# Optimization experiments

Measured on AMD Instinct MI355X. Metric: run time of the kernel, lower is better.

The kernel has to match this reference:

```python
import jax, jax.numpy as jnp
import numpy as np

N_NODES = 100000
N_EDGES = 1600000
NFEAT, NHID, NCLASS = 128, 64, 40
NLAYERS = 4
P = 2.0


def setup_inputs() -> dict:
    key = jax.random.key(0)
    ks = jax.random.split(key, 10)
    x = jax.random.normal(ks[0], (N_NODES, NFEAT), dtype=jnp.float32)
    edge_index = jax.random.randint(ks[1], (2, N_EDGES), 0, N_NODES, dtype=jnp.int32)
    s_in = 1.0 / np.sqrt(NFEAT)
    s_h = 1.0 / np.sqrt(NHID)
    return {
        "x": x,
        "edge_index": edge_index,
        "enc_W": jax.random.normal(ks[2], (NHID, NFEAT), dtype=jnp.float32) * s_in,
        "enc_b": jnp.zeros((NHID,), dtype=jnp.float32),
        "conv_W": jax.random.normal(ks[3], (NHID, NHID), dtype=jnp.float32) * s_h,
        "conv_b": jnp.zeros((NHID,), dtype=jnp.float32),
        "W_skip": jax.random.normal(ks[4], (NHID, NHID), dtype=jnp.float32) * s_h,
        "dec_W": jax.random.normal(ks[5], (NCLASS, NHID), dtype=jnp.float32) * s_h,
        "dec_b": jnp.zeros((NCLASS,), dtype=jnp.float32),
    }


def _gcn_conv(X, W, b, src, dst, n):
    # PyG GCNConv: add self-loops, symmetric normalization, then X @ W^T + b
    H = X @ W.T  # [n, nhid]
    ones = jnp.ones_like(dst, dtype=X.dtype)
    deg = jax.ops.segment_sum(ones, dst, num_segments=n)  # in-degree incl. self loops
    dinv = jnp.where(deg > 0, jax.lax.rsqrt(deg), 0.0)
    norm = dinv[src] * dinv[dst]  # [E+n]
    out = jax.ops.segment_sum(norm[:, None] * H[src], dst, num_segments=n)
    return out + b


def _gamma(X, row, col, n, p):
    # G2 gating: scatter-mean over edges of sum |X[row]-X[col]|^p, then tanh.
    # (conv_gg output in the original G2 is dead code and omitted.)
    diff = jnp.sum(jnp.abs(X[row] - X[col]) ** p, axis=-1)  # [E]
    s = jax.ops.segment_sum(diff, row, num_segments=n)
    cnt = jax.ops.segment_sum(jnp.ones_like(diff), row, num_segments=n)
    return jnp.tanh(s / jnp.maximum(cnt, 1.0))  # [n]


def reference(x, edge_index, enc_W, enc_b, conv_W, conv_b, W_skip, dec_W, dec_b):
    n = x.shape[0]
    row, col = edge_index[0], edge_index[1]
    # self-loop augmented edges for GCNConv
    loop = jnp.arange(n, dtype=edge_index.dtype)
    src_sl = jnp.concatenate([row, loop])
    dst_sl = jnp.concatenate([col, loop])

    X = jax.nn.relu(x @ enc_W.T + enc_b)  # [n, nhid]
    X_init = X
    skip_val = X_init @ W_skip.T  # constant across layers

    for _ in range(NLAYERS):
        X_agg = jax.nn.relu(_gcn_conv(X, conv_W, conv_b, src_sl, dst_sl, n))
        g = _gamma(X, row, col, n, P)[:, None]  # gamma_smooth == gamma_squash (dead convs)
        denom = 1.0 + g + g
        A = 1.0 / denom
        B = g / denom
        C = g / denom
        X = A * X + B * X_agg + C * skip_val

    return X @ dec_W.T + dec_b  # [n, nclass]
```

## Files before the change

### kernel.cpp

```cpp
#include <hip/hip_runtime.h>
#include <hip/hip_bf16.h>

#define NFEAT 128
#define NHID  64
#define NCLASS 40
#define NLAYERS 4


__global__ void count_rank_k(const int* __restrict__ ei, int E,
                             int* __restrict__ cnt_col, int* __restrict__ cnt_row,
                             int* __restrict__ rank) {
    int t = blockIdx.x * blockDim.x + threadIdx.x;
    int base = t * 4;
    if (base >= E) return;
    if (base + 4 <= E) {
        int4 c4 = *reinterpret_cast<const int4*>(ei + E + base);
        int4 r4 = *reinterpret_cast<const int4*>(ei + base);
        int4 k4;
        k4.x = atomicAdd(&cnt_col[c4.x], 1);
        k4.y = atomicAdd(&cnt_col[c4.y], 1);
        k4.z = atomicAdd(&cnt_col[c4.z], 1);
        k4.w = atomicAdd(&cnt_col[c4.w], 1);
        atomicAdd(&cnt_row[r4.x], 1);
        atomicAdd(&cnt_row[r4.y], 1);
        atomicAdd(&cnt_row[r4.z], 1);
        atomicAdd(&cnt_row[r4.w], 1);
        *reinterpret_cast<int4*>(rank + base) = k4;
    } else {
        for (int e = base; e < E; ++e) {
            rank[e] = atomicAdd(&cnt_col[ei[E + e]], 1);
            atomicAdd(&cnt_row[ei[e]], 1);
        }
    }
}

__global__ void scanA_k(const int* __restrict__ cnt, int* __restrict__ off,
                        int* __restrict__ bsum, float* __restrict__ dinv, int n) {
    __shared__ int t[1024];
    int i = blockIdx.x * 1024 + threadIdx.x;
    int x = (i < n) ? cnt[i] : 0;
    if (i < n) dinv[i] = 1.0f / sqrtf((float)(x + 1));
    t[threadIdx.x] = x;
    __syncthreads();
    for (int d = 1; d < 1024; d <<= 1) {
        int y = (threadIdx.x >= (unsigned)d) ? t[threadIdx.x - d] : 0;
        __syncthreads();
        t[threadIdx.x] += y;
        __syncthreads();
    }
    if (i < n) off[i] = t[threadIdx.x] - x;
    if (threadIdx.x == 1023) bsum[blockIdx.x] = t[1023];
}

__global__ void scanB_k(int* __restrict__ bsum, int nb) {
    __shared__ int t[1024];
    int x = (threadIdx.x < (unsigned)nb) ? bsum[threadIdx.x] : 0;
    t[threadIdx.x] = x;
    __syncthreads();
    for (int d = 1; d < 1024; d <<= 1) {
        int y = (threadIdx.x >= (unsigned)d) ? t[threadIdx.x - d] : 0;
        __syncthreads();
        t[threadIdx.x] += y;
        __syncthreads();
    }
    if (threadIdx.x < (unsigned)nb) bsum[threadIdx.x] = t[threadIdx.x] - x;
}

__global__ void scanC_k(int* __restrict__ off, const int* __restrict__ bsum,
                        float* __restrict__ gs, int n, int total) {
    int i = blockIdx.x * 1024 + threadIdx.x;
    if (i < n) {
        off[i] += bsum[blockIdx.x];
        gs[i] = 0.f;
    }
    if (i == 0) off[n] = total;
}

__global__ void scatter_k(const int* __restrict__ ei, int E,
                          const int* __restrict__ col_off, const int* __restrict__ rank,
                          int* __restrict__ csr) {
    int t = blockIdx.x * blockDim.x + threadIdx.x;
    int base = t * 8;
    if (base >= E) return;
    if (base + 8 <= E) {
        int4 rA = *reinterpret_cast<const int4*>(ei + base);
        int4 rB = *reinterpret_cast<const int4*>(ei + base + 4);
        int4 cA = *reinterpret_cast<const int4*>(ei + E + base);
        int4 cB = *reinterpret_cast<const int4*>(ei + E + base + 4);
        int4 kA = *reinterpret_cast<const int4*>(rank + base);
        int4 kB = *reinterpret_cast<const int4*>(rank + base + 4);
        csr[col_off[cA.x] + kA.x] = rA.x;
        csr[col_off[cA.y] + kA.y] = rA.y;
        csr[col_off[cA.z] + kA.z] = rA.z;
        csr[col_off[cA.w] + kA.w] = rA.w;
        csr[col_off[cB.x] + kB.x] = rB.x;
        csr[col_off[cB.y] + kB.y] = rB.y;
        csr[col_off[cB.z] + kB.z] = rB.z;
        csr[col_off[cB.w] + kB.w] = rB.w;
    } else {
        for (int e = base; e < E; ++e)
            csr[col_off[ei[E + e]] + rank[e]] = ei[e];
    }
}


template<int K, int M, bool RELU, bool BIAS>
__global__ void dense_small_k(const float* __restrict__ A, const float* __restrict__ W,
                              const float* __restrict__ b, float* __restrict__ out, int n) {
    int v = blockIdx.x * blockDim.x + threadIdx.x;
    if (v >= n) return;
    float a[K];
    const float4* ap = reinterpret_cast<const float4*>(A + (size_t)v * K);
#pragma unroll
    for (int k = 0; k < K / 4; ++k) {
        float4 t = ap[k];
        a[4 * k + 0] = t.x; a[4 * k + 1] = t.y; a[4 * k + 2] = t.z; a[4 * k + 3] = t.w;
    }
    float4* op = reinterpret_cast<float4*>(out + (size_t)v * M);
#pragma unroll 1
    for (int m = 0; m < M; m += 4) {
        float acc0 = BIAS ? b[m + 0] : 0.f;
        float acc1 = BIAS ? b[m + 1] : 0.f;
        float acc2 = BIAS ? b[m + 2] : 0.f;
        float acc3 = BIAS ? b[m + 3] : 0.f;
#pragma unroll
        for (int k = 0; k < K; ++k) {
            float av = a[k];
            acc0 = fmaf(av, W[(m + 0) * K + k], acc0);
            acc1 = fmaf(av, W[(m + 1) * K + k], acc1);
            acc2 = fmaf(av, W[(m + 2) * K + k], acc2);
            acc3 = fmaf(av, W[(m + 3) * K + k], acc3);
        }
        if (RELU) {
            acc0 = fmaxf(acc0, 0.f); acc1 = fmaxf(acc1, 0.f);
            acc2 = fmaxf(acc2, 0.f); acc3 = fmaxf(acc3, 0.f);
        }
        float4 o; o.x = acc0; o.y = acc1; o.z = acc2; o.w = acc3;
        op[m >> 2] = o;
    }
}


template<int K, int M, int MC>
__global__ void dense_enc_k(const float* __restrict__ A, const float* __restrict__ W,
                            const float* __restrict__ b, float* __restrict__ out, int n) {
    int v = blockIdx.x * blockDim.x + threadIdx.x;
    if (v >= n) return;
    const float4* ap = reinterpret_cast<const float4*>(A + (size_t)v * K);
    float4* op = reinterpret_cast<float4*>(out + (size_t)v * M);
#pragma unroll 1
    for (int mc = 0; mc < M; mc += MC) {
        float acc[MC];
#pragma unroll
        for (int m = 0; m < MC; ++m) acc[m] = b[mc + m];
#pragma unroll 1
        for (int kb = 0; kb < K / 4; ++kb) {
            float4 a4 = ap[kb];
#pragma unroll
            for (int m = 0; m < MC; ++m) {
                const float* wr = W + (size_t)(mc + m) * K + kb * 4;
                acc[m] = fmaf(a4.x, wr[0], acc[m]);
                acc[m] = fmaf(a4.y, wr[1], acc[m]);
                acc[m] = fmaf(a4.z, wr[2], acc[m]);
                acc[m] = fmaf(a4.w, wr[3], acc[m]);
            }
        }
#pragma unroll
        for (int m = 0; m < MC; m += 4) {
            float4 o;
            o.x = fmaxf(acc[m + 0], 0.f);
            o.y = fmaxf(acc[m + 1], 0.f);
            o.z = fmaxf(acc[m + 2], 0.f);
            o.w = fmaxf(acc[m + 3], 0.f);
            op[(mc + m) >> 2] = o;
        }
    }
}

__global__ void gather_k(const float* __restrict__ X, const int* __restrict__ csr,
                         const int* __restrict__ col_off, const float* __restrict__ dinv,
                         float* __restrict__ pre, float* __restrict__ gs, int n) {
    int v = blockIdx.x * 4 + (threadIdx.x >> 6);
    if (v >= n) return;
    int lane = threadIdx.x & 63;
    int grp = lane >> 4;
    int sub = lane & 15;

    float4 xv = reinterpret_cast<const float4*>(X + (size_t)v * NHID)[sub];
    int beg = col_off[v], end = col_off[v + 1];

    float4 acc = make_float4(0.f, 0.f, 0.f, 0.f);
    int e = beg + grp;
    for (; e + 4 < end; e += 8) {
        int s0 = csr[e];
        int s1 = csr[e + 4];
        float w0 = dinv[s0];
        float w1 = dinv[s1];
        float4 x0 = reinterpret_cast<const float4*>(X + (size_t)s0 * NHID)[sub];
        float4 x1 = reinterpret_cast<const float4*>(X + (size_t)s1 * NHID)[sub];
        acc.x = fmaf(w0, x0.x, acc.x); acc.y = fmaf(w0, x0.y, acc.y);
        acc.z = fmaf(w0, x0.z, acc.z); acc.w = fmaf(w0, x0.w, acc.w);
        acc.x = fmaf(w1, x1.x, acc.x); acc.y = fmaf(w1, x1.y, acc.y);
        acc.z = fmaf(w1, x1.z, acc.z); acc.w = fmaf(w1, x1.w, acc.w);
        float dx = x0.x - xv.x; float p0 = dx * dx;
        dx = x0.y - xv.y; p0 = fmaf(dx, dx, p0);
        dx = x0.z - xv.z; p0 = fmaf(dx, dx, p0);
        dx = x0.w - xv.w; p0 = fmaf(dx, dx, p0);
        dx = x1.x - xv.x; float p1 = dx * dx;
        dx = x1.y - xv.y; p1 = fmaf(dx, dx, p1);
        dx = x1.z - xv.z; p1 = fmaf(dx, dx, p1);
        dx = x1.w - xv.w; p1 = fmaf(dx, dx, p1);
#pragma unroll
        for (int m = 1; m <= 8; m <<= 1) {
            p0 += __shfl_xor(p0, m, 64);
            p1 += __shfl_xor(p1, m, 64);
        }
        if (sub == 0) {
            atomicAdd(&gs[s0], p0);
            atomicAdd(&gs[s1], p1);
        }
    }
    if (e < end) {
        int s = csr[e];
        float w = dinv[s];
        float4 xs = reinterpret_cast<const float4*>(X + (size_t)s * NHID)[sub];
        acc.x = fmaf(w, xs.x, acc.x); acc.y = fmaf(w, xs.y, acc.y);
        acc.z = fmaf(w, xs.z, acc.z); acc.w = fmaf(w, xs.w, acc.w);
        float dx = xs.x - xv.x; float part = dx * dx;
        dx = xs.y - xv.y; part = fmaf(dx, dx, part);
        dx = xs.z - xv.z; part = fmaf(dx, dx, part);
        dx = xs.w - xv.w; part = fmaf(dx, dx, part);
#pragma unroll
        for (int m = 1; m <= 8; m <<= 1) part += __shfl_xor(part, m, 64);
        if (sub == 0) atomicAdd(&gs[s], part);
    }
#pragma unroll
    for (int m = 16; m <= 32; m <<= 1) {
        acc.x += __shfl_xor(acc.x, m, 64);
        acc.y += __shfl_xor(acc.y, m, 64);
        acc.z += __shfl_xor(acc.z, m, 64);
        acc.w += __shfl_xor(acc.w, m, 64);
    }
    if (grp == 0) {
        float dv = dinv[v];
        float dv2 = dv * dv;
        float4 o;
        o.x = fmaf(dv, acc.x, dv2 * xv.x);
        o.y = fmaf(dv, acc.y, dv2 * xv.y);
        o.z = fmaf(dv, acc.z, dv2 * xv.z);
        o.w = fmaf(dv, acc.w, dv2 * xv.w);
        reinterpret_cast<float4*>(pre + (size_t)v * NHID)[sub] = o;
    }
}

__global__ void update_k(float* __restrict__ X, const float* __restrict__ pre,
                         const float* __restrict__ skip, const float* __restrict__ W,
                         const float* __restrict__ b, float* __restrict__ gs,
                         const int* __restrict__ cnt_row, int n) {
    int v = blockIdx.x * blockDim.x + threadIdx.x;
    if (v >= n) return;
    float a[NHID];
    const float4* ap = reinterpret_cast<const float4*>(pre + (size_t)v * NHID);
#pragma unroll
    for (int k = 0; k < NHID / 4; ++k) {
        float4 t = ap[k];
        a[4 * k + 0] = t.x; a[4 * k + 1] = t.y; a[4 * k + 2] = t.z; a[4 * k + 3] = t.w;
    }
    float gv = tanhf(gs[v] / fmaxf((float)cnt_row[v], 1.f));
    gs[v] = 0.f;
    float inv = 1.0f / (1.0f + 2.0f * gv);

    float4* Xp = reinterpret_cast<float4*>(X + (size_t)v * NHID);
    const float4* Sp = reinterpret_cast<const float4*>(skip + (size_t)v * NHID);
#pragma unroll 1
    for (int m = 0; m < NHID; m += 4) {
        float t0 = b[m + 0], t1 = b[m + 1], t2 = b[m + 2], t3 = b[m + 3];
#pragma unroll
        for (int k = 0; k < NHID; ++k) {
            float av = a[k];
            t0 = fmaf(av, W[(m + 0) * NHID + k], t0);
            t1 = fmaf(av, W[(m + 1) * NHID + k], t1);
            t2 = fmaf(av, W[(m + 2) * NHID + k], t2);
            t3 = fmaf(av, W[(m + 3) * NHID + k], t3);
        }
        t0 = fmaxf(t0, 0.f); t1 = fmaxf(t1, 0.f);
        t2 = fmaxf(t2, 0.f); t3 = fmaxf(t3, 0.f);
        float4 x4 = Xp[m >> 2];
        float4 s4 = Sp[m >> 2];
        float4 o;
        o.x = (x4.x + gv * (t0 + s4.x)) * inv;
        o.y = (x4.y + gv * (t1 + s4.y)) * inv;
        o.z = (x4.z + gv * (t2 + s4.z)) * inv;
        o.w = (x4.w + gv * (t3 + s4.w)) * inv;
        Xp[m >> 2] = o;
    }
}


extern "C" void kernel_launch(void* const* d_in, const int* in_sizes, int n_in,
                              void* d_out, int out_size, void* d_ws, size_t ws_size,
                              hipStream_t stream) {
    const float* x      = (const float*)d_in[0];
    const int*   ei     = (const int*)  d_in[1];
    const float* enc_W  = (const float*)d_in[2];
    const float* enc_b  = (const float*)d_in[3];
    const float* conv_W = (const float*)d_in[4];
    const float* conv_b = (const float*)d_in[5];
    const float* W_skip = (const float*)d_in[6];
    const float* dec_W  = (const float*)d_in[7];
    const float* dec_b  = (const float*)d_in[8];

    const int n = in_sizes[0] / NFEAT;
    const int E = in_sizes[1] / 2;

    char* ws = (char*)d_ws;
    auto alloc = [&](size_t bytes) {
        char* p = ws;
        ws += (bytes + 255) & ~(size_t)255;
        return p;
    };

    float* X    = (float*)alloc((size_t)n * NHID * 4);
    float* pre  = (float*)alloc((size_t)n * NHID * 4);
    float* skip = (float*)alloc((size_t)n * NHID * 4);
    float* gs   = (float*)alloc((size_t)n * 4);
    float* dinv = (float*)alloc((size_t)n * 4);
    int* cnt_row = (int*)alloc((size_t)n * 4);
    int* cnt_col = (int*)alloc((size_t)n * 4);
    int* col_off = (int*)alloc((size_t)(n + 1) * 4);
    int* rank    = (int*)alloc((size_t)E * 4);
    int* bsc     = (int*)alloc(1024 * 4);
    int* csr     = (int*)alloc((size_t)E * 4);

    hipMemsetAsync(cnt_row, 0, (size_t)n * 4, stream);
    hipMemsetAsync(cnt_col, 0, (size_t)n * 4, stream);

    count_rank_k<<<(E / 4 + 255) / 256, 256, 0, stream>>>(ei, E, cnt_col, cnt_row, rank);

    int nb = (n + 1023) / 1024;
    scanA_k<<<nb, 1024, 0, stream>>>(cnt_col, col_off, bsc, dinv, n);
    scanB_k<<<1, 1024, 0, stream>>>(bsc, nb);
    scanC_k<<<nb, 1024, 0, stream>>>(col_off, bsc, gs, n, E);
    scatter_k<<<(E / 8 + 255) / 256, 256, 0, stream>>>(ei, E, col_off, rank, csr);

    dense_enc_k<NFEAT, NHID, 32><<<(n + 255) / 256, 256, 0, stream>>>(x, enc_W, enc_b, X, n);
    dense_small_k<NHID, NHID, false, false><<<(n + 255) / 256, 256, 0, stream>>>(X, W_skip, nullptr, skip, n);

    for (int l = 0; l < NLAYERS; ++l) {
        gather_k<<<(n + 3) / 4, 256, 0, stream>>>(X, csr, col_off, dinv, pre, gs, n);
        update_k<<<(n + 255) / 256, 256, 0, stream>>>(X, pre, skip, conv_W, conv_b, gs, cnt_row, n);
    }

    dense_small_k<NHID, NCLASS, false, true><<<(n + 255) / 256, 256, 0, stream>>>(X, dec_W, dec_b, (float*)d_out, n);
}
```

Measured before the change: 966.4 us.

## Gather neighbor features from a bf16 shadow copy of X

Keeps a bf16 copy of the node features, written by the encoder and update kernels, and has the edge gather kernel read neighbor rows from it instead of fp32. This halves the bytes fetched per random neighbor access in the memory-bound aggregation and gamma computation. The cost is extra bf16 writes and reduced precision in the aggregation and in the squared-difference gating term. The edge-count kernel also processes eight edges per thread instead of four.

```diff
diff --git a/kernel.cpp b/kernel.cpp
--- a/kernel.cpp
+++ b/kernel.cpp
@@ -6,26 +6,46 @@
 #define NCLASS 40
 #define NLAYERS 4
 
+static __device__ __forceinline__ unsigned short f2bf(float f) {
+    unsigned u = __float_as_uint(f);
+    unsigned r = (u + 0x7FFF + ((u >> 16) & 1)) >> 16;
+    return (unsigned short)r;
+}
+static __device__ __forceinline__ float bf2f(unsigned short h) {
+    return __uint_as_float((unsigned)h << 16);
+}
+
 
 __global__ void count_rank_k(const int* __restrict__ ei, int E,
                              int* __restrict__ cnt_col, int* __restrict__ cnt_row,
                              int* __restrict__ rank) {
     int t = blockIdx.x * blockDim.x + threadIdx.x;
-    int base = t * 4;
+    int base = t * 8;
     if (base >= E) return;
-    if (base + 4 <= E) {
-        int4 c4 = *reinterpret_cast<const int4*>(ei + E + base);
-        int4 r4 = *reinterpret_cast<const int4*>(ei + base);
-        int4 k4;
-        k4.x = atomicAdd(&cnt_col[c4.x], 1);
-        k4.y = atomicAdd(&cnt_col[c4.y], 1);
-        k4.z = atomicAdd(&cnt_col[c4.z], 1);
-        k4.w = atomicAdd(&cnt_col[c4.w], 1);
-        atomicAdd(&cnt_row[r4.x], 1);
-        atomicAdd(&cnt_row[r4.y], 1);
-        atomicAdd(&cnt_row[r4.z], 1);
-        atomicAdd(&cnt_row[r4.w], 1);
-        *reinterpret_cast<int4*>(rank + base) = k4;
+    if (base + 8 <= E) {
+        int4 cA = *reinterpret_cast<const int4*>(ei + E + base);
+        int4 cB = *reinterpret_cast<const int4*>(ei + E + base + 4);
+        int4 rA = *reinterpret_cast<const int4*>(ei + base);
+        int4 rB = *reinterpret_cast<const int4*>(ei + base + 4);
+        int4 kA, kB;
+        kA.x = atomicAdd(&cnt_col[cA.x], 1);
+        kA.y = atomicAdd(&cnt_col[cA.y], 1);
+        kA.z = atomicAdd(&cnt_col[cA.z], 1);
+        kA.w = atomicAdd(&cnt_col[cA.w], 1);
+        kB.x = atomicAdd(&cnt_col[cB.x], 1);
+        kB.y = atomicAdd(&cnt_col[cB.y], 1);
+        kB.z = atomicAdd(&cnt_col[cB.z], 1);
+        kB.w = atomicAdd(&cnt_col[cB.w], 1);
+        atomicAdd(&cnt_row[rA.x], 1);
+        atomicAdd(&cnt_row[rA.y], 1);
+        atomicAdd(&cnt_row[rA.z], 1);
+        atomicAdd(&cnt_row[rA.w], 1);
+        atomicAdd(&cnt_row[rB.x], 1);
+        atomicAdd(&cnt_row[rB.y], 1);
+        atomicAdd(&cnt_row[rB.z], 1);
+        atomicAdd(&cnt_row[rB.w], 1);
+        *reinterpret_cast<int4*>(rank + base) = kA;
+        *reinterpret_cast<int4*>(rank + base + 4) = kB;
     } else {
         for (int e = base; e < E; ++e) {
             rank[e] = atomicAdd(&cnt_col[ei[E + e]], 1);
@@ -143,11 +163,13 @@
 
 template<int K, int M, int MC>
 __global__ void dense_enc_k(const float* __restrict__ A, const float* __restrict__ W,
-                            const float* __restrict__ b, float* __restrict__ out, int n) {
+                            const float* __restrict__ b, float* __restrict__ out,
+                            unsigned short* __restrict__ out16, int n) {
     int v = blockIdx.x * blockDim.x + threadIdx.x;
     if (v >= n) return;
     const float4* ap = reinterpret_cast<const float4*>(A + (size_t)v * K);
     float4* op = reinterpret_cast<float4*>(out + (size_t)v * M);
+    ushort4* hp = reinterpret_cast<ushort4*>(out16 + (size_t)v * M);
 #pragma unroll 1
     for (int mc = 0; mc < M; mc += MC) {
         float acc[MC];
@@ -173,11 +195,14 @@
             o.z = fmaxf(acc[m + 2], 0.f);
             o.w = fmaxf(acc[m + 3], 0.f);
             op[(mc + m) >> 2] = o;
-        }
-    }
-}
-
-__global__ void gather_k(const float* __restrict__ X, const int* __restrict__ csr,
+            ushort4 h;
+            h.x = f2bf(o.x); h.y = f2bf(o.y); h.z = f2bf(o.z); h.w = f2bf(o.w);
+            hp[(mc + m) >> 2] = h;
+        }
+    }
+}
+
+__global__ void gather_k(const unsigned short* __restrict__ X16, const int* __restrict__ csr,
                          const int* __restrict__ col_off, const float* __restrict__ dinv,
                          float* __restrict__ pre, float* __restrict__ gs, int n) {
     int v = blockIdx.x * 4 + (threadIdx.x >> 6);
@@ -186,7 +211,9 @@
     int grp = lane >> 4;
     int sub = lane & 15;
 
-    float4 xv = reinterpret_cast<const float4*>(X + (size_t)v * NHID)[sub];
+    ushort4 hv = reinterpret_cast<const ushort4*>(X16 + (size_t)v * NHID)[sub];
+    float4 xv;
+    xv.x = bf2f(hv.x); xv.y = bf2f(hv.y); xv.z = bf2f(hv.z); xv.w = bf2f(hv.w);
     int beg = col_off[v], end = col_off[v + 1];
 
     float4 acc = make_float4(0.f, 0.f, 0.f, 0.f);
@@ -196,8 +223,11 @@
         int s1 = csr[e + 4];
         float w0 = dinv[s0];
         float w1 = dinv[s1];
-        float4 x0 = reinterpret_cast<const float4*>(X + (size_t)s0 * NHID)[sub];
-        float4 x1 = reinterpret_cast<const float4*>(X + (size_t)s1 * NHID)[sub];
+        ushort4 h0 = reinterpret_cast<const ushort4*>(X16 + (size_t)s0 * NHID)[sub];
+        ushort4 h1 = reinterpret_cast<const ushort4*>(X16 + (size_t)s1 * NHID)[sub];
+        float4 x0, x1;
+        x0.x = bf2f(h0.x); x0.y = bf2f(h0.y); x0.z = bf2f(h0.z); x0.w = bf2f(h0.w);
+        x1.x = bf2f(h1.x); x1.y = bf2f(h1.y); x1.z = bf2f(h1.z); x1.w = bf2f(h1.w);
         acc.x = fmaf(w0, x0.x, acc.x); acc.y = fmaf(w0, x0.y, acc.y);
         acc.z = fmaf(w0, x0.z, acc.z); acc.w = fmaf(w0, x0.w, acc.w);
         acc.x = fmaf(w1, x1.x, acc.x); acc.y = fmaf(w1, x1.y, acc.y);
@@ -223,7 +253,9 @@
     if (e < end) {
         int s = csr[e];
         float w = dinv[s];
-        float4 xs = reinterpret_cast<const float4*>(X + (size_t)s * NHID)[sub];
+        ushort4 hs = reinterpret_cast<const ushort4*>(X16 + (size_t)s * NHID)[sub];
+        float4 xs;
+        xs.x = bf2f(hs.x); xs.y = bf2f(hs.y); xs.z = bf2f(hs.z); xs.w = bf2f(hs.w);
         acc.x = fmaf(w, xs.x, acc.x); acc.y = fmaf(w, xs.y, acc.y);
         acc.z = fmaf(w, xs.z, acc.z); acc.w = fmaf(w, xs.w, acc.w);
         float dx = xs.x - xv.x; float part = dx * dx;
@@ -253,7 +285,8 @@
     }
 }
 
-__global__ void update_k(float* __restrict__ X, const float* __restrict__ pre,
+__global__ void update_k(float* __restrict__ X, unsigned short* __restrict__ X16,
+                         const float* __restrict__ pre,
                          const float* __restrict__ skip, const float* __restrict__ W,
                          const float* __restrict__ b, float* __restrict__ gs,
                          const int* __restrict__ cnt_row, int n) {
@@ -271,6 +304,7 @@
     float inv = 1.0f / (1.0f + 2.0f * gv);
 
     float4* Xp = reinterpret_cast<float4*>(X + (size_t)v * NHID);
+    ushort4* Hp = reinterpret_cast<ushort4*>(X16 + (size_t)v * NHID);
     const float4* Sp = reinterpret_cast<const float4*>(skip + (size_t)v * NHID);
 #pragma unroll 1
     for (int m = 0; m < NHID; m += 4) {
@@ -293,6 +327,9 @@
         o.z = (x4.z + gv * (t2 + s4.z)) * inv;
         o.w = (x4.w + gv * (t3 + s4.w)) * inv;
         Xp[m >> 2] = o;
+        ushort4 h;
+        h.x = f2bf(o.x); h.y = f2bf(o.y); h.z = f2bf(o.z); h.w = f2bf(o.w);
+        Hp[m >> 2] = h;
     }
 }
 
@@ -321,6 +358,7 @@
     };
 
     float* X    = (float*)alloc((size_t)n * NHID * 4);
+    unsigned short* X16 = (unsigned short*)alloc((size_t)n * NHID * 2);
     float* pre  = (float*)alloc((size_t)n * NHID * 4);
     float* skip = (float*)alloc((size_t)n * NHID * 4);
     float* gs   = (float*)alloc((size_t)n * 4);
@@ -335,7 +373,7 @@
     hipMemsetAsync(cnt_row, 0, (size_t)n * 4, stream);
     hipMemsetAsync(cnt_col, 0, (size_t)n * 4, stream);
 
-    count_rank_k<<<(E / 4 + 255) / 256, 256, 0, stream>>>(ei, E, cnt_col, cnt_row, rank);
+    count_rank_k<<<(E / 8 + 255) / 256, 256, 0, stream>>>(ei, E, cnt_col, cnt_row, rank);
 
     int nb = (n + 1023) / 1024;
     scanA_k<<<nb, 1024, 0, stream>>>(cnt_col, col_off, bsc, dinv, n);
@@ -343,12 +381,12 @@
     scanC_k<<<nb, 1024, 0, stream>>>(col_off, bsc, gs, n, E);
     scatter_k<<<(E / 8 + 255) / 256, 256, 0, stream>>>(ei, E, col_off, rank, csr);
 
-    dense_enc_k<NFEAT, NHID, 32><<<(n + 255) / 256, 256, 0, stream>>>(x, enc_W, enc_b, X, n);
+    dense_enc_k<NFEAT, NHID, 32><<<(n + 255) / 256, 256, 0, stream>>>(x, enc_W, enc_b, X, X16, n);
     dense_small_k<NHID, NHID, false, false><<<(n + 255) / 256, 256, 0, stream>>>(X, W_skip, nullptr, skip, n);
 
     for (int l = 0; l < NLAYERS; ++l) {
-        gather_k<<<(n + 3) / 4, 256, 0, stream>>>(X, csr, col_off, dinv, pre, gs, n);
-        update_k<<<(n + 255) / 256, 256, 0, stream>>>(X, pre, skip, conv_W, conv_b, gs, cnt_row, n);
+        gather_k<<<(n + 3) / 4, 256, 0, stream>>>(X16, csr, col_off, dinv, pre, gs, n);
+        update_k<<<(n + 255) / 256, 256, 0, stream>>>(X, X16, pre, skip, conv_W, conv_b, gs, cnt_row, n);
     }
 
     dense_small_k<NHID, NCLASS, false, true><<<(n + 255) / 256, 256, 0, stream>>>(X, dec_W, dec_b, (float*)d_out, n);
```

Result: slower. 1.058 ms (+9.5%).

## Assign one 16-lane group per node with grid-stride loop; move row counting to scatter

Applied to the files above, without the earlier changes.

The gather kernel now gives each node to a 16-lane group instead of a full 64-lane wavefront, with a persistent grid of 2048 blocks walking nodes in a grid-stride loop and unrolling edges by 4. This drops the cross-group shuffle reduction and the idle lanes on low-degree nodes, at the cost of less parallelism within each node and more divergence between groups of the same wavefront. The row-degree atomics move from count_rank_k into scatter_k, which spreads the atomic traffic across two kernels.

```diff
diff --git a/kernel.cpp b/kernel.cpp
--- a/kernel.cpp
+++ b/kernel.cpp
@@ -8,29 +8,21 @@
 
 
 __global__ void count_rank_k(const int* __restrict__ ei, int E,
-                             int* __restrict__ cnt_col, int* __restrict__ cnt_row,
-                             int* __restrict__ rank) {
+                             int* __restrict__ cnt_col, int* __restrict__ rank) {
     int t = blockIdx.x * blockDim.x + threadIdx.x;
     int base = t * 4;
     if (base >= E) return;
     if (base + 4 <= E) {
         int4 c4 = *reinterpret_cast<const int4*>(ei + E + base);
-        int4 r4 = *reinterpret_cast<const int4*>(ei + base);
         int4 k4;
         k4.x = atomicAdd(&cnt_col[c4.x], 1);
         k4.y = atomicAdd(&cnt_col[c4.y], 1);
         k4.z = atomicAdd(&cnt_col[c4.z], 1);
         k4.w = atomicAdd(&cnt_col[c4.w], 1);
-        atomicAdd(&cnt_row[r4.x], 1);
-        atomicAdd(&cnt_row[r4.y], 1);
-        atomicAdd(&cnt_row[r4.z], 1);
-        atomicAdd(&cnt_row[r4.w], 1);
         *reinterpret_cast<int4*>(rank + base) = k4;
     } else {
-        for (int e = base; e < E; ++e) {
+        for (int e = base; e < E; ++e)
             rank[e] = atomicAdd(&cnt_col[ei[E + e]], 1);
-            atomicAdd(&cnt_row[ei[e]], 1);
-        }
     }
 }
 
@@ -78,7 +70,7 @@
 
 __global__ void scatter_k(const int* __restrict__ ei, int E,
                           const int* __restrict__ col_off, const int* __restrict__ rank,
-                          int* __restrict__ csr) {
+                          int* __restrict__ cnt_row, int* __restrict__ csr) {
     int t = blockIdx.x * blockDim.x + threadIdx.x;
     int base = t * 8;
     if (base >= E) return;
@@ -89,6 +81,14 @@
         int4 cB = *reinterpret_cast<const int4*>(ei + E + base + 4);
         int4 kA = *reinterpret_cast<const int4*>(rank + base);
         int4 kB = *reinterpret_cast<const int4*>(rank + base + 4);
+        atomicAdd(&cnt_row[rA.x], 1);
+        atomicAdd(&cnt_row[rA.y], 1);
+        atomicAdd(&cnt_row[rA.z], 1);
+        atomicAdd(&cnt_row[rA.w], 1);
+        atomicAdd(&cnt_row[rB.x], 1);
+        atomicAdd(&cnt_row[rB.y], 1);
+        atomicAdd(&cnt_row[rB.z], 1);
+        atomicAdd(&cnt_row[rB.w], 1);
         csr[col_off[cA.x] + kA.x] = rA.x;
         csr[col_off[cA.y] + kA.y] = rA.y;
         csr[col_off[cA.z] + kA.z] = rA.z;
@@ -98,8 +98,10 @@
         csr[col_off[cB.z] + kB.z] = rB.z;
         csr[col_off[cB.w] + kB.w] = rB.w;
     } else {
-        for (int e = base; e < E; ++e)
+        for (int e = base; e < E; ++e) {
+            atomicAdd(&cnt_row[ei[e]], 1);
             csr[col_off[ei[E + e]] + rank[e]] = ei[e];
+        }
     }
 }
 
@@ -180,68 +182,74 @@
 __global__ void gather_k(const float* __restrict__ X, const int* __restrict__ csr,
                          const int* __restrict__ col_off, const float* __restrict__ dinv,
                          float* __restrict__ pre, float* __restrict__ gs, int n) {
-    int v = blockIdx.x * 4 + (threadIdx.x >> 6);
-    if (v >= n) return;
-    int lane = threadIdx.x & 63;
-    int grp = lane >> 4;
-    int sub = lane & 15;
-
-    float4 xv = reinterpret_cast<const float4*>(X + (size_t)v * NHID)[sub];
-    int beg = col_off[v], end = col_off[v + 1];
-
-    float4 acc = make_float4(0.f, 0.f, 0.f, 0.f);
-    int e = beg + grp;
-    for (; e + 4 < end; e += 8) {
-        int s0 = csr[e];
-        int s1 = csr[e + 4];
-        float w0 = dinv[s0];
-        float w1 = dinv[s1];
-        float4 x0 = reinterpret_cast<const float4*>(X + (size_t)s0 * NHID)[sub];
-        float4 x1 = reinterpret_cast<const float4*>(X + (size_t)s1 * NHID)[sub];
-        acc.x = fmaf(w0, x0.x, acc.x); acc.y = fmaf(w0, x0.y, acc.y);
-        acc.z = fmaf(w0, x0.z, acc.z); acc.w = fmaf(w0, x0.w, acc.w);
-        acc.x = fmaf(w1, x1.x, acc.x); acc.y = fmaf(w1, x1.y, acc.y);
-        acc.z = fmaf(w1, x1.z, acc.z); acc.w = fmaf(w1, x1.w, acc.w);
-        float dx = x0.x - xv.x; float p0 = dx * dx;
-        dx = x0.y - xv.y; p0 = fmaf(dx, dx, p0);
-        dx = x0.z - xv.z; p0 = fmaf(dx, dx, p0);
-        dx = x0.w - xv.w; p0 = fmaf(dx, dx, p0);
-        dx = x1.x - xv.x; float p1 = dx * dx;
-        dx = x1.y - xv.y; p1 = fmaf(dx, dx, p1);
-        dx = x1.z - xv.z; p1 = fmaf(dx, dx, p1);
-        dx = x1.w - xv.w; p1 = fmaf(dx, dx, p1);
-#pragma unroll
-        for (int m = 1; m <= 8; m <<= 1) {
-            p0 += __shfl_xor(p0, m, 64);
-            p1 += __shfl_xor(p1, m, 64);
-        }
-        if (sub == 0) {
-            atomicAdd(&gs[s0], p0);
-            atomicAdd(&gs[s1], p1);
-        }
-    }
-    if (e < end) {
-        int s = csr[e];
-        float w = dinv[s];
-        float4 xs = reinterpret_cast<const float4*>(X + (size_t)s * NHID)[sub];
-        acc.x = fmaf(w, xs.x, acc.x); acc.y = fmaf(w, xs.y, acc.y);
-        acc.z = fmaf(w, xs.z, acc.z); acc.w = fmaf(w, xs.w, acc.w);
-        float dx = xs.x - xv.x; float part = dx * dx;
-        dx = xs.y - xv.y; part = fmaf(dx, dx, part);
-        dx = xs.z - xv.z; part = fmaf(dx, dx, part);
-        dx = xs.w - xv.w; part = fmaf(dx, dx, part);
-#pragma unroll
-        for (int m = 1; m <= 8; m <<= 1) part += __shfl_xor(part, m, 64);
-        if (sub == 0) atomicAdd(&gs[s], part);
-    }
-#pragma unroll
-    for (int m = 16; m <= 32; m <<= 1) {
-        acc.x += __shfl_xor(acc.x, m, 64);
-        acc.y += __shfl_xor(acc.y, m, 64);
-        acc.z += __shfl_xor(acc.z, m, 64);
-        acc.w += __shfl_xor(acc.w, m, 64);
-    }
-    if (grp == 0) {
+    int gid = (blockIdx.x * blockDim.x + threadIdx.x) >> 4;
+    int ngrp = (gridDim.x * blockDim.x) >> 4;
+    int sub = threadIdx.x & 15;
+
+    for (int v = gid; v < n; v += ngrp) {
+        float4 xv = reinterpret_cast<const float4*>(X + (size_t)v * NHID)[sub];
+        int beg = col_off[v], end = col_off[v + 1];
+        float4 acc = make_float4(0.f, 0.f, 0.f, 0.f);
+        int e = beg;
+        for (; e + 4 <= end; e += 4) {
+            int s0 = csr[e], s1 = csr[e + 1], s2 = csr[e + 2], s3 = csr[e + 3];
+            float w0 = dinv[s0], w1 = dinv[s1], w2 = dinv[s2], w3 = dinv[s3];
+            float4 x0 = reinterpret_cast<const float4*>(X + (size_t)s0 * NHID)[sub];
+            float4 x1 = reinterpret_cast<const float4*>(X + (size_t)s1 * NHID)[sub];
+            float4 x2 = reinterpret_cast<const float4*>(X + (size_t)s2 * NHID)[sub];
+            float4 x3 = reinterpret_cast<const float4*>(X + (size_t)s3 * NHID)[sub];
+            acc.x = fmaf(w0, x0.x, acc.x); acc.y = fmaf(w0, x0.y, acc.y);
+            acc.z = fmaf(w0, x0.z, acc.z); acc.w = fmaf(w0, x0.w, acc.w);
+            acc.x = fmaf(w1, x1.x, acc.x); acc.y = fmaf(w1, x1.y, acc.y);
+            acc.z = fmaf(w1, x1.z, acc.z); acc.w = fmaf(w1, x1.w, acc.w);
+            acc.x = fmaf(w2, x2.x, acc.x); acc.y = fmaf(w2, x2.y, acc.y);
+            acc.z = fmaf(w2, x2.z, acc.z); acc.w = fmaf(w2, x2.w, acc.w);
+            acc.x = fmaf(w3, x3.x, acc.x); acc.y = fmaf(w3, x3.y, acc.y);
+            acc.z = fmaf(w3, x3.z, acc.z); acc.w = fmaf(w3, x3.w, acc.w);
+            float dx = x0.x - xv.x; float p0 = dx * dx;
+            dx = x0.y - xv.y; p0 = fmaf(dx, dx, p0);
+            dx = x0.z - xv.z; p0 = fmaf(dx, dx, p0);
+            dx = x0.w - xv.w; p0 = fmaf(dx, dx, p0);
+            dx = x1.x - xv.x; float p1 = dx * dx;
+            dx = x1.y - xv.y; p1 = fmaf(dx, dx, p1);
+            dx = x1.z - xv.z; p1 = fmaf(dx, dx, p1);
+            dx = x1.w - xv.w; p1 = fmaf(dx, dx, p1);
+            dx = x2.x - xv.x; float p2 = dx * dx;
+            dx = x2.y - xv.y; p2 = fmaf(dx, dx, p2);
+            dx = x2.z - xv.z; p2 = fmaf(dx, dx, p2);
+            dx = x2.w - xv.w; p2 = fmaf(dx, dx, p2);
+            dx = x3.x - xv.x; float p3 = dx * dx;
+            dx = x3.y - xv.y; p3 = fmaf(dx, dx, p3);
+            dx = x3.z - xv.z; p3 = fmaf(dx, dx, p3);
+            dx = x3.w - xv.w; p3 = fmaf(dx, dx, p3);
+#pragma unroll
+            for (int m = 1; m <= 8; m <<= 1) {
+                p0 += __shfl_xor(p0, m, 64);
+                p1 += __shfl_xor(p1, m, 64);
+                p2 += __shfl_xor(p2, m, 64);
+                p3 += __shfl_xor(p3, m, 64);
+            }
+            if (sub == 0) {
+                atomicAdd(&gs[s0], p0);
+                atomicAdd(&gs[s1], p1);
+                atomicAdd(&gs[s2], p2);
+                atomicAdd(&gs[s3], p3);
+            }
+        }
+        for (; e < end; ++e) {
+            int s = csr[e];
+            float w = dinv[s];
+            float4 xs = reinterpret_cast<const float4*>(X + (size_t)s * NHID)[sub];
+            acc.x = fmaf(w, xs.x, acc.x); acc.y = fmaf(w, xs.y, acc.y);
+            acc.z = fmaf(w, xs.z, acc.z); acc.w = fmaf(w, xs.w, acc.w);
+            float dx = xs.x - xv.x; float part = dx * dx;
+            dx = xs.y - xv.y; part = fmaf(dx, dx, part);
+            dx = xs.z - xv.z; part = fmaf(dx, dx, part);
+            dx = xs.w - xv.w; part = fmaf(dx, dx, part);
+#pragma unroll
+            for (int m = 1; m <= 8; m <<= 1) part += __shfl_xor(part, m, 64);
+            if (sub == 0) atomicAdd(&gs[s], part);
+        }
         float dv = dinv[v];
         float dv2 = dv * dv;
         float4 o;
@@ -335,19 +343,19 @@
     hipMemsetAsync(cnt_row, 0, (size_t)n * 4, stream);
     hipMemsetAsync(cnt_col, 0, (size_t)n * 4, stream);
 
-    count_rank_k<<<(E / 4 + 255) / 256, 256, 0, stream>>>(ei, E, cnt_col, cnt_row, rank);
+    count_rank_k<<<(E / 4 + 255) / 256, 256, 0, stream>>>(ei, E, cnt_col, rank);
 
     int nb = (n + 1023) / 1024;
     scanA_k<<<nb, 1024, 0, stream>>>(cnt_col, col_off, bsc, dinv, n);
     scanB_k<<<1, 1024, 0, stream>>>(bsc, nb);
     scanC_k<<<nb, 1024, 0, stream>>>(col_off, bsc, gs, n, E);
-    scatter_k<<<(E / 8 + 255) / 256, 256, 0, stream>>>(ei, E, col_off, rank, csr);
+    scatter_k<<<(E / 8 + 255) / 256, 256, 0, stream>>>(ei, E, col_off, rank, cnt_row, csr);
 
     dense_enc_k<NFEAT, NHID, 32><<<(n + 255) / 256, 256, 0, stream>>>(x, enc_W, enc_b, X, n);
     dense_small_k<NHID, NHID, false, false><<<(n + 255) / 256, 256, 0, stream>>>(X, W_skip, nullptr, skip, n);
 
     for (int l = 0; l < NLAYERS; ++l) {
-        gather_k<<<(n + 3) / 4, 256, 0, stream>>>(X, csr, col_off, dinv, pre, gs, n);
+        gather_k<<<2048, 256, 0, stream>>>(X, csr, col_off, dinv, pre, gs, n);
         update_k<<<(n + 255) / 256, 256, 0, stream>>>(X, pre, skip, conv_W, conv_b, gs, cnt_row, n);
     }
 
```

New measurement: 994.2 us. +2.9%, slower.
